# Optimization experiments

Measured on AMD Instinct MI355X. Metric: run time of the kernel, lower is better.

Reference implementation:

```python
import jax, jax.numpy as jnp
import numpy as np

MIN_DIST = 4
BASE_PRIMES = np.array([2, 3, 5, 7])  # A, C, G, U
# canonical pair prime products: AU=2*7=14, CG=3*5=15, GU=5*7=35


def nussinov(s):
    """Nussinov max-score non-crossing pairing: O(N^3) DP (vectorized per
    anti-diagonal) + stack-based traceback. s: [N,N] float64, symmetric, >=0.
    Returns symmetric 0/1 pair mask. Mirrors kirigami.nussinov (CPU numpy)."""
    N = s.shape[0]
    D = np.zeros((N, N))  # D[d, i] = dp[i, i+d]
    E = np.zeros((N, N))  # E[d, j] = dp[j-d, j]
    ar = np.arange(N)
    for d in range(1, N):
        m = N - d
        pair = (D[d - 2, 1:m + 1] if d >= 2 else 0.0) + s[ar[:m], ar[:m] + d]
        # split over k=i..j-1: dp[i,k] + dp[k+1,j] (k=i covers i-unpaired)
        split = (D[0:d, 0:m] + E[d - 1::-1, d:N]).max(axis=0)
        val = np.maximum(pair, split)
        D[d, :m] = val
        E[d, d:] = val
    dp = np.zeros((N, N))
    for d in range(1, N):
        dp[ar[:N - d], ar[:N - d] + d] = D[d, :N - d]
    eps = 1e-9
    pm = np.zeros((N, N))
    stack = [(0, N - 1)]
    while stack:
        i, j = stack.pop()
        if j <= i:
            continue
        v = dp[i, j]
        if v <= eps:
            continue
        if dp[i + 1, j] >= v - eps:
            stack.append((i + 1, j))
        elif s[i, j] > 0 and dp[i + 1, j - 1] + s[i, j] >= v - eps:
            pm[i, j] = pm[j, i] = 1.0
            stack.append((i + 1, j - 1))
        else:
            ks = np.arange(i, j)
            k = int(ks[np.argmax(dp[i, ks] + dp[ks + 1, j])])
            stack.append((i, k))
            stack.append((k + 1, j))
    return pm


def _premask(con, feat):
    """Symmetrize + remove sharp angles (tril(-4)+triu(4)) + canonical-pair mask."""
    c = con[0, 0]                      # [N, N]
    c = (c + c.T) * 0.5                # Symmetrize
    N = c.shape[0]
    idx = jnp.arange(N)
    dist_ok = jnp.abs(idx[:, None] - idx[None, :]) >= MIN_DIST  # RemoveSharp
    seq = feat[0, :4, :, 0]            # [4, N] one-hot base encoding
    primes = jnp.asarray(BASE_PRIMES)[jnp.argmax(seq, axis=0)]  # [N]
    prod = primes[:, None] * primes[None, :]
    canon = (prod == 14) | (prod == 15) | (prod == 35)          # Canonicalize
    return c * (dist_ok & canon)


def setup_inputs() -> dict:
    key = jax.random.key(0)
    k1, k2 = jax.random.split(key)
    N = 1024
    con = jax.random.uniform(k1, (1, 1, N, N), dtype=jnp.float32)
    feat = jax.random.normal(k2, (1, 16, N, N), dtype=jnp.float32)
    return {"con": con, "feat": feat}


def reference(con, feat):
    c = _premask(con, feat)
    # original: GPU->CPU numpy float64 DP, then mask back on device
    mask = nussinov(np.asarray(c, dtype=np.float64))
    out = c * jnp.asarray(mask, dtype=c.dtype)
    return out.reshape(con.shape)
```

## Files before the change

### kernel.cpp

```cpp
#include <hip/hip_runtime.h>

#define NN 1024
#define BT 32
#define TT 32
#define NTILES ((TT * (TT + 1)) / 2)

__device__ __forceinline__ double gload_cc(const double* p) {
    double v;
    asm volatile("global_load_dwordx2 %0, %1, off sc0 sc1" : "=v"(v) : "v"(p));
    return v;
}
__device__ __forceinline__ void gstore_cc(double* p, double v) {
    asm volatile("global_store_dwordx2 %0, %1, off sc0 sc1" :: "v"(p), "v"(v));
}
__device__ __forceinline__ void gstore_flag(int* p, int v) {
    asm volatile("global_store_dword %0, %1, off sc0 sc1" :: "v"(p), "v"(v));
}
#define VWAIT0 asm volatile("s_waitcnt vmcnt(0)" ::: "memory")

__device__ __forceinline__ void waitflag2(const int* f, int a0, int b0, int a1, int b1) {
    const int* p0 = &f[(a0 * TT + b0) << 4];
    const int* p1 = &f[(a1 * TT + b1) << 4];
    int it = 0;
    while (true) {
        int v0, v1;
        asm volatile("global_load_dword %0, %2, off sc0 sc1\n\t"
                     "global_load_dword %1, %3, off sc0 sc1\n\t"
                     "s_waitcnt vmcnt(0)"
                     : "=&v"(v0), "=&v"(v1)
                     : "v"(p0), "v"(p1));
        if (v0 & v1) break;
        if (it < 8) __builtin_amdgcn_s_sleep(1);
        else        __builtin_amdgcn_s_sleep(15);
        ++it;
    }
    asm volatile("" ::: "memory");
}
__device__ __forceinline__ void waitflag4(const int* f, int a0, int b0, int a1, int b1,
                                          int a2, int b2, int a3, int b3) {
    const int* p0 = &f[(a0 * TT + b0) << 4];
    const int* p1 = &f[(a1 * TT + b1) << 4];
    const int* p2 = &f[(a2 * TT + b2) << 4];
    const int* p3 = &f[(a3 * TT + b3) << 4];
    int it = 0;
    while (true) {
        int v0, v1, v2, v3;
        asm volatile("global_load_dword %0, %4, off sc0 sc1\n\t"
                     "global_load_dword %1, %5, off sc0 sc1\n\t"
                     "global_load_dword %2, %6, off sc0 sc1\n\t"
                     "global_load_dword %3, %7, off sc0 sc1\n\t"
                     "s_waitcnt vmcnt(0)"
                     : "=&v"(v0), "=&v"(v1), "=&v"(v2), "=&v"(v3)
                     : "v"(p0), "v"(p1), "v"(p2), "v"(p3));
        if (v0 & v1 & v2 & v3) break;
        if (it < 8) __builtin_amdgcn_s_sleep(1);
        else        __builtin_amdgcn_s_sleep(15);
        ++it;
    }
    asm volatile("" ::: "memory");
}
__device__ __forceinline__ void waitflag2_blk(const int* f, int a0, int b0, int a1, int b1) {
    if (threadIdx.x < 64) waitflag2(f, a0, b0, a1, b1);
    __syncthreads();
}
__device__ __forceinline__ void waitflag4_blk(const int* f, int a0, int b0, int a1, int b1,
                                              int a2, int b2, int a3, int b3) {
    if (threadIdx.x < 64) waitflag4(f, a0, b0, a1, b1, a2, b2, a3, b3);
    __syncthreads();
}

__global__ void primes_kernel(const float* __restrict__ feat, int* __restrict__ primes) {
    int i = blockIdx.x * blockDim.x + threadIdx.x;
    if (i < NN) {
        float best = feat[i * NN];
        int arg = 0;
        for (int ch = 1; ch < 4; ++ch) {
            float v = feat[ch * NN * NN + i * NN];
            if (v > best) { best = v; arg = ch; }
        }
        const int P[4] = {2, 3, 5, 7};
        primes[i] = P[arg];
    }
}

__global__ void prep_kernel(const float* __restrict__ con, const int* __restrict__ primes,
                            float* __restrict__ S, double* __restrict__ R,
                            double* __restrict__ C, float* __restrict__ out,
                            int* __restrict__ flags,
                            int* __restrict__ qi, int* __restrict__ qj,
                            int* __restrict__ qready, int* __restrict__ qctl) {
    int idx = blockIdx.x * blockDim.x + threadIdx.x;
    int i = idx >> 10;
    int j = idx & (NN - 1);
    float c = (con[idx] + con[j * NN + i]) * 0.5f;
    int prod = primes[i] * primes[j];
    bool canon = (prod == 14) | (prod == 15) | (prod == 35);
    int d = i - j; if (d < 0) d = -d;
    S[idx] = (canon && d >= 4) ? c : 0.0f;
    R[idx] = 0.0;
    C[idx] = 0.0;
    out[idx] = 0.0f;
    if (idx < TT * TT * 16) flags[idx] = 0;
    if (idx < 4096) qready[idx] = (idx == 0) ? 1 : 0;
    if (idx == 0) {
        qi[0] = 0; qj[0] = NN - 1;
        qctl[0] = 0;
        qctl[16] = 1;
        qctl[32] = 1;
    }
}

__global__ __launch_bounds__(256) void nuss_tiles_kernel(double* __restrict__ R,
                                                         double* __restrict__ C,
                                                         const float* __restrict__ S,
                                                         int* __restrict__ flags) {
    __shared__ double DJJc[32][33];
    __shared__ double Vtc[32][33];
    __shared__ __attribute__((aligned(16))) double Ast[32][34];
    __shared__ __attribute__((aligned(16))) double Bst[32][34];
    __shared__ double Pld[32][33];
    __shared__ float  Sld[32][32];
    __shared__ double edgeCol[33];
    __shared__ double Prt[2][4][32];

    int b = blockIdx.x, dd = 0;
    while (b >= TT - dd) { b -= TT - dd; ++dd; }
    const int I = b, J = b + dd;
    const int aI = I * BT, aJ = J * BT;
    const int tid = threadIdx.x;
    const int wid = tid >> 6;
    const int lane = tid & 63;
    const int r = lane >> 1;
    const int h = lane & 1;

    if (dd == 0) {
        #pragma unroll
        for (int w = 0; w < 4; ++w) {
            int idx = w * 256 + tid; int rr = idx >> 5, cc = idx & 31;
            Sld[rr][cc] = S[(aI + rr) * NN + aI + cc];
        }
        for (int idx = tid; idx < 32 * 33; idx += 256)
            ((double*)Vtc)[idx] = 0.0;
        __syncthreads();
        if (wid == 0) {
            double vrow[16];
            #pragma unroll
            for (int u = 0; u < 16; ++u) vrow[u] = 0.0;
            for (int s = 1; s <= 31; ++s) {
                int c = r + s;
                bool act = (c <= 31);
                double acc = 0.0;
                if (act) {
                    double t0 = 0.0, t1 = 0.0, t2 = 0.0, t3 = 0.0;
                    #pragma unroll
                    for (int u = 0; u < 16; u += 4) {
                        int k0 = h * 16 + u;
                        t0 = fmax(t0, vrow[u]     + Vtc[c][k0 + 1]);
                        t1 = fmax(t1, vrow[u + 1] + Vtc[c][k0 + 2]);
                        t2 = fmax(t2, vrow[u + 2] + Vtc[c][k0 + 3]);
                        t3 = fmax(t3, vrow[u + 3] + Vtc[c][k0 + 4]);
                    }
                    acc = fmax(fmax(t0, t1), fmax(t2, t3));
                }
                acc = fmax(acc, __shfl_xor(acc, 1));
                if (act) {
                    double best = fmax(acc, Vtc[c - 1][r + 1] + (double)Sld[r][c]);
                    if (h == 0) Vtc[c][r] = best;
                    #pragma unroll
                    for (int u = 0; u < 16; ++u)
                        if (h * 16 + u == c) vrow[u] = best;
                }
            }
        }
        __syncthreads();
        #pragma unroll
        for (int w = 0; w < 4; ++w) {
            int idx = w * 256 + tid; int rr = idx >> 5, cc = idx & 31;
            gstore_cc(&R[(aI + rr) * NN + aI + cc], Vtc[cc][rr]);
        }
        #pragma unroll
        for (int w = 0; w < 4; ++w) {
            int idx = w * 256 + tid; int cc = idx >> 5, rr = idx & 31;
            gstore_cc(&C[(aI + cc) * NN + aI + rr], Vtc[cc][rr]);
        }
        VWAIT0;
        __syncthreads();
        if (tid == 0) gstore_flag(&flags[(I * TT + I) << 4], 1);
        return;
    }

    const int nk = dd - 1;
    const int off = (wid & 1) * 16 + h * 8;
    waitflag2_blk(flags, I, I, J, J);

    double ra[4], rb[4];
    double ec = 0.0, ve = 0.0;
    double asl[8];
    double ar1 = 0.0;
    #pragma unroll
    for (int w = 0; w < 4; ++w) {
        int idx = w * 256 + tid; int cc = idx >> 5, mm = idx & 31;
        ra[w] = gload_cc(&C[(aJ + cc) * NN + aJ + mm]);
    }
    if (wid < 2) {
        #pragma unroll
        for (int u = 0; u < 8; ++u)
            asl[u] = gload_cc(&R[(aI + r) * NN + aI + off + u]);
    }
    if (r < 31) ar1 = gload_cc(&R[(aI + r) * NN + aI + r + 1]);
    if (wid == 0 && nk == 0) {
        if (lane < 33) ec = gload_cc(&R[(aI + lane) * NN + (aJ - 1)]);
        if (lane < 32) ve = gload_cc(&R[(aI + 32) * NN + aJ + lane]);
    }
    #pragma unroll
    for (int w = 0; w < 4; ++w) {
        int idx = w * 256 + tid; int rr = idx >> 5, cc = idx & 31;
        Sld[rr][cc] = S[(aI + rr) * NN + aJ + cc];
    }
    for (int idx = tid; idx < 32 * 33; idx += 256)
        ((double*)Vtc)[idx] = 0.0;
    VWAIT0;
    #pragma unroll
    for (int w = 0; w < 4; ++w) {
        int idx = w * 256 + tid; int cc = idx >> 5, mm = idx & 31;
        DJJc[cc][mm] = ra[w];
    }
    if (tid < 32) DJJc[tid][32] = 0.0;
    double slice8[8];
    if (wid < 2) {
        #pragma unroll
        for (int u = 0; u < 8; ++u)
            slice8[u] = (off + u > r + 1) ? asl[u] : -1.0e30;
    } else {
        #pragma unroll
        for (int u = 0; u < 8; ++u) slice8[u] = 0.0;
    }
    if (wid == 0 && nk == 0) {
        if (lane < 33) edgeCol[lane] = ec;
        if (lane < 32) Vtc[lane][32] = ve;
    }
    __syncthreads();

    double P[16];
    #pragma unroll
    for (int x = 0; x < 16; ++x) P[x] = 0.0;
    const int rg = lane >> 3, cg = lane & 7;
    const int r4 = rg * 4, c4 = cg * 4;

    auto kkloop = [&]() {
        for (int kk = wid * 8; kk < wid * 8 + 8; ++kk) {
            double2 av0 = *(const double2*)&Ast[kk][r4];
            double2 av1 = *(const double2*)&Ast[kk][r4 + 2];
            double2 bv0 = *(const double2*)&Bst[kk][c4];
            double2 bv1 = *(const double2*)&Bst[kk][c4 + 2];
            P[0]  = fmax(P[0],  av0.x + bv0.x); P[1]  = fmax(P[1],  av0.x + bv0.y);
            P[2]  = fmax(P[2],  av0.x + bv1.x); P[3]  = fmax(P[3],  av0.x + bv1.y);
            P[4]  = fmax(P[4],  av0.y + bv0.x); P[5]  = fmax(P[5],  av0.y + bv0.y);
            P[6]  = fmax(P[6],  av0.y + bv1.x); P[7]  = fmax(P[7],  av0.y + bv1.y);
            P[8]  = fmax(P[8],  av1.x + bv0.x); P[9]  = fmax(P[9],  av1.x + bv0.y);
            P[10] = fmax(P[10], av1.x + bv1.x); P[11] = fmax(P[11], av1.x + bv1.y);
            P[12] = fmax(P[12], av1.y + bv0.x); P[13] = fmax(P[13], av1.y + bv0.y);
            P[14] = fmax(P[14], av1.y + bv1.x); P[15] = fmax(P[15], av1.y + bv1.y);
        }
    };
    auto proc = [&](int t1, int t2, bool last) {
        if (t2 >= 0) waitflag4_blk(flags, I, t1, t1, J, I, t2, t2, J);
        else         waitflag2_blk(flags, I, t1, t1, J);
        if (last && wid == 0) {
            if (lane < 33) ec = gload_cc(&R[(aI + lane) * NN + (aJ - 1)]);
            if (lane < 32) ve = gload_cc(&R[(aI + 32) * NN + aJ + lane]);
        }
        int k1 = t1 * BT;
        #pragma unroll
        for (int w = 0; w < 4; ++w) {
            int idx = w * 256 + tid; int rr = idx >> 5, kk = idx & 31;
            ra[w] = gload_cc(&R[(aI + rr) * NN + k1 + kk]);
            rb[w] = gload_cc(&C[(aJ + rr) * NN + k1 + 1 + kk]);
        }
        VWAIT0;
        #pragma unroll
        for (int w = 0; w < 4; ++w) {
            int idx = w * 256 + tid; int rr = idx >> 5, kk = idx & 31;
            Ast[kk][rr] = ra[w];
            Bst[kk][rr] = rb[w];
        }
        if (last && wid == 0) {
            if (lane < 33) edgeCol[lane] = ec;
            if (lane < 32) Vtc[lane][32] = ve;
        }
        __syncthreads();
        if (t2 >= 0) {
            int k2 = t2 * BT;
            #pragma unroll
            for (int w = 0; w < 4; ++w) {
                int idx = w * 256 + tid; int rr = idx >> 5, kk = idx & 31;
                ra[w] = gload_cc(&R[(aI + rr) * NN + k2 + kk]);
                rb[w] = gload_cc(&C[(aJ + rr) * NN + k2 + 1 + kk]);
            }
        }
        kkloop();
        if (t2 >= 0) {
            __syncthreads();
            VWAIT0;
            #pragma unroll
            for (int w = 0; w < 4; ++w) {
                int idx = w * 256 + tid; int rr = idx >> 5, kk = idx & 31;
                Ast[kk][rr] = ra[w];
                Bst[kk][rr] = rb[w];
            }
            __syncthreads();
            kkloop();
        }
        __syncthreads();
    };

    {
        int tl = (I + J) >> 1, tr = ((I + J) >> 1) + 1;
        int pend = -1;
        for (int q = 0; q < nk; ++q) {
            int t;
            if ((q & 1) == 0) { if (tl >= I + 1) t = tl--; else t = tr++; }
            else              { if (tr <= J - 1) t = tr++; else t = tl--; }
            if (pend < 0) { pend = t; continue; }
            int rp = (pend - I > J - pend) ? pend - I : J - pend;
            int rt = (t - I > J - t) ? t - I : J - t;
            if (rp == rt) { proc(pend, t, q == nk - 1); pend = -1; }
            else          { proc(pend, -1, false); pend = t; }
        }
        if (pend >= 0) proc(pend, -1, true);
    }

    if (nk > 0) {
        if (wid == 0) {
            #pragma unroll
            for (int x = 0; x < 4; ++x)
                #pragma unroll
                for (int y = 0; y < 4; ++y)
                    Pld[r4 + x][c4 + y] = P[x * 4 + y];
        }
        __syncthreads();
        if (wid == 1) {
            #pragma unroll
            for (int x = 0; x < 4; ++x)
                #pragma unroll
                for (int y = 0; y < 4; ++y)
                    Pld[r4 + x][c4 + y] = fmax(Pld[r4 + x][c4 + y], P[x * 4 + y]);
        }
        __syncthreads();
        if (wid == 2) {
            #pragma unroll
            for (int x = 0; x < 4; ++x)
                #pragma unroll
                for (int y = 0; y < 4; ++y)
                    Pld[r4 + x][c4 + y] = fmax(Pld[r4 + x][c4 + y], P[x * 4 + y]);
        }
        __syncthreads();
        if (wid == 3) {
            #pragma unroll
            for (int x = 0; x < 4; ++x)
                #pragma unroll
                for (int y = 0; y < 4; ++y)
                    Pld[r4 + x][c4 + y] = fmax(Pld[r4 + x][c4 + y], P[x * 4 + y]);
        }
        __syncthreads();
    } else {
        for (int idx = tid; idx < 32 * 33; idx += 256)
            ((double*)Pld)[idx] = 0.0;
        __syncthreads();
    }

    {
        const double* bsel = (wid < 2) ? &Vtc[0][0] : &DJJc[0][0];
        double ecr = edgeCol[r];
        double ecp = edgeCol[r + 1];
        double pA[8], pB[8];
        double p1 = 0.0, p2 = 0.0, shc = 0.0, shp = 0.0, erc = 0.0, erp = 0.0;

#define PREFQ(PV, SS)                                                 \
    { int cq_ = (r + (SS) - 31) & 31;                                 \
      const double* bp_ = bsel + cq_ * 33 + off + 1;                  \
      _Pragma("unroll")                                               \
      for (int u = 0; u < 8; ++u) PV[u] = bp_[u]; }

#define STEPQ(PV, SS, BUF)                                            \
    { int c_ = r + (SS) - 31;                                         \
      bool act_ = ((unsigned)c_ < 32u);                               \
      int cc_ = c_ & 31;                                              \
      double t0_ = fmax(slice8[0] + PV[0], slice8[1] + PV[1]);        \
      double t1_ = fmax(slice8[2] + PV[2], slice8[3] + PV[3]);        \
      double t2_ = fmax(slice8[4] + PV[4], slice8[5] + PV[5]);        \
      double t3_ = fmax(slice8[6] + PV[6], slice8[7] + PV[7]);        \
      double pa_ = fmax(fmax(t0_, t1_), fmax(t2_, t3_));              \
      pa_ = fmax(pa_, __shfl_xor(pa_, 1));                            \
      if (h == 0) Prt[BUF][wid][r] = pa_;                             \
      __syncthreads();                                                \
      double a0_ = Prt[BUF][0][r];                                    \
      double a1_ = Prt[BUF][1][r];                                    \
      double a2_ = Prt[BUF][2][r];                                    \
      double a3_ = Prt[BUF][3][r];                                    \
      double er_  = Vtc[cc_][32];                                     \
      double dj0_ = DJJc[cc_][0];                                     \
      double pld_ = Pld[r][cc_];                                      \
      float  sld_ = Sld[r][cc_];                                      \
      shp = shc; erp = erc; erc = er_;                                \
      shc = __shfl_down(p1, 2);                                       \
      double shd_ = __shfl_down(p2, 4);                               \
      p2 = p1;                                                        \
      double acc_ = fmax(fmax(a0_, a1_), fmax(a2_, a3_));             \
      if (act_) {                                                     \
          double best_ = acc_;                                        \
          best_ = fmax(best_, (r == 31) ? erc : shc);                 \
          if (r < 31)                                                 \
              best_ = fmax(best_, ar1 + ((r == 30) ? erc : shd_));    \
          best_ = fmax(best_, ecr + dj0_);                            \
          best_ = fmax(best_, pld_);                                  \
          double pv_ = (c_ == 0) ? ecp : ((r == 31) ? erp : shp);     \
          best_ = fmax(best_, pv_ + (double)sld_);                    \
          if (wid == 0 && h == 0) Vtc[c_][r] = best_;                 \
          if (wid >= 2) {                                             \
              _Pragma("unroll")                                       \
              for (int u = 0; u < 8; ++u)                             \
                  if (off + u == c_) slice8[u] = best_;               \
          }                                                           \
          p1 = best_;                                                 \
      } }

        PREFQ(pA, 0)
        PREFQ(pB, 1)
        for (int s2 = 0; s2 < 64; s2 += 2) {
            STEPQ(pA, s2, 0)
            PREFQ(pA, s2 + 2)
            STEPQ(pB, s2 + 1, 1)
            PREFQ(pB, s2 + 3)
        }
#undef PREFQ
#undef STEPQ
    }
    __syncthreads();

    #pragma unroll
    for (int w = 0; w < 4; ++w) {
        int idx = w * 256 + tid; int rr = idx >> 5, cc = idx & 31;
        gstore_cc(&R[(aI + rr) * NN + aJ + cc], Vtc[cc][rr]);
    }
    #pragma unroll
    for (int w = 0; w < 4; ++w) {
        int idx = w * 256 + tid; int cc = idx >> 5, rr = idx & 31;
        gstore_cc(&C[(aJ + cc) * NN + aI + rr], Vtc[cc][rr]);
    }
    VWAIT0;
    __syncthreads();
    if (tid == 0) gstore_flag(&flags[(I * TT + J) << 4], 1);
}

__global__ __launch_bounds__(256) void traceback_kernel(const double* __restrict__ R,
                                                        const double* __restrict__ C,
                                                        const float* __restrict__ S,
                                                        float* __restrict__ out,
                                                        int* __restrict__ qi,
                                                        int* __restrict__ qj,
                                                        int* __restrict__ qready,
                                                        int* __restrict__ qctl) {
    __shared__ double Rw[16][17];
    __shared__ float  Sw[16][17];
    __shared__ int sh_cmd, sh_i, sh_j;
    __shared__ double sred_v[4];
    __shared__ int sred_k[4];
    const double eps = 1e-9;
    const int tid = threadIdx.x;
    int* headp = qctl;
    int* tailp = qctl + 16;
    int* pendp = qctl + 32;

    int i = 0, j = 0; double v = 0.0;
    bool have = false;
    int ai = -(1 << 29), aj = 0;
    int myidx = -1;

    while (true) {
        if (tid == 0) {
            int cmd;
            int guard = 0;
            while (true) {
                if (!have) {
                    if (++guard > (1 << 22)) { cmd = -1; break; }
                    if (myidx < 0) myidx = atomicAdd(headp, 1);
                    int rdy = 0;
                    if (myidx < 4096)
                        rdy = __hip_atomic_load(&qready[myidx], __ATOMIC_RELAXED,
                                                __HIP_MEMORY_SCOPE_AGENT);
                    if (rdy) {
                        int ni, nj;
                        asm volatile("global_load_dword %0, %2, off sc0 sc1\n\t"
                                     "global_load_dword %1, %3, off sc0 sc1\n\t"
                                     "s_waitcnt vmcnt(0)"
                                     : "=&v"(ni), "=&v"(nj)
                                     : "v"(&qi[myidx]), "v"(&qj[myidx]));
                        myidx = -1;
                        i = ni; j = nj;
                        if (j <= i) { atomicAdd(pendp, -1); continue; }
                        v = R[i * NN + j];
                        if (v <= eps) { atomicAdd(pendp, -1); continue; }
                        have = true;
                        continue;
                    }
                    int pend = __hip_atomic_load(pendp, __ATOMIC_RELAXED,
                                                 __HIP_MEMORY_SCOPE_AGENT);
                    if (pend == 0) { cmd = -1; break; }
                    __builtin_amdgcn_s_sleep(2);
                    continue;
                }
                int u = i - ai, w = aj - j;
                if ((unsigned)u > 15u || (unsigned)w > 14u) { cmd = 1; break; }
                double a = Rw[u][w];
                if (a >= v - eps) {
                    ++i; v = a;
                    if (j <= i || v <= eps) { have = false; atomicAdd(pendp, -1); }
                    continue;
                }
                float sv = Sw[u][w];
                double b2 = Rw[u][w + 1];
                if (sv > 0.0f && b2 + (double)sv >= v - eps) {
                    out[i * NN + j] = sv; out[j * NN + i] = sv;
                    ++i; --j; v = b2;
                    if (j <= i || v <= eps) { have = false; atomicAdd(pendp, -1); }
                    continue;
                }
                cmd = 0; break;
            }
            sh_cmd = cmd; sh_i = i; sh_j = j;
        }
        __syncthreads();
        int cmd = sh_cmd;
        if (cmd < 0) break;

        if (cmd == 1) {
            int i0 = sh_i, j0 = sh_j;
            int di = tid >> 4, dj = tid & 15;
            int rr = i0 + 1 + di; if (rr > NN - 1) rr = NN - 1;
            int cc = j0 - dj;     if (cc < 0) cc = 0;
            Rw[di][dj] = R[rr * NN + cc];
            int sr = i0 + di;     if (sr > NN - 1) sr = NN - 1;
            Sw[di][dj] = S[sr * NN + cc];
            __syncthreads();
            if (tid == 0) { ai = i0; aj = j0; }
            continue;
        }

        const int si = sh_i, sj = sh_j;
        double bv = -1.0; int bk = 0x7fffffff;
        for (int k = si + tid; k < sj; k += 256) {
            double tv = R[si * NN + k] + C[sj * NN + k + 1];
            if (tv > bv) { bv = tv; bk = k; }
        }
        for (int offr = 32; offr; offr >>= 1) {
            double ov = __shfl_down(bv, offr);
            int    ok = __shfl_down(bk, offr);
            if (ov > bv || (ov == bv && ok < bk)) { bv = ov; bk = ok; }
        }
        if ((tid & 63) == 0) { sred_v[tid >> 6] = bv; sred_k[tid >> 6] = bk; }
        __syncthreads();
        if (tid == 0) {
            double fv = sred_v[0]; int fk = sred_k[0];
            for (int w = 1; w < 4; ++w)
                if (sred_v[w] > fv || (sred_v[w] == fv && sred_k[w] < fk)) { fv = sred_v[w]; fk = sred_k[w]; }
            int slot = atomicAdd(tailp, 1);
            int rv = fk + 1;
            asm volatile("global_store_dword %0, %1, off sc0 sc1" :: "v"(&qi[slot]), "v"(rv));
            asm volatile("global_store_dword %0, %1, off sc0 sc1" :: "v"(&qj[slot]), "v"(sj));
            VWAIT0;
            atomicAdd(pendp, 1);
            VWAIT0;
            gstore_flag(&qready[slot], 1);
            j = fk;
            if (j <= i) { have = false; atomicAdd(pendp, -1); }
            else {
                v = R[i * NN + j];
                if (v <= eps) { have = false; atomicAdd(pendp, -1); }
                else have = true;
            }
        }
        __syncthreads();
    }
}

extern "C" void kernel_launch(void* const* d_in, const int* in_sizes, int n_in,
                              void* d_out, int out_size, void* d_ws, size_t ws_size,
                              hipStream_t stream) {
    const float* con  = (const float*)d_in[0];
    const float* feat = (const float*)d_in[1];
    float* out = (float*)d_out;

    char* ws = (char*)d_ws;
    double* R      = (double*)(ws);
    double* C      = (double*)(ws + (size_t)8  * 1024 * 1024);
    float*  S      = (float*) (ws + (size_t)16 * 1024 * 1024);
    int*    primes = (int*)   (ws + (size_t)20 * 1024 * 1024);
    int*    flags  = (int*)   (ws + (size_t)20 * 1024 * 1024 + 8192);
    char*   qbase  = ws + (size_t)20 * 1024 * 1024 + 128 * 1024;
    int*    qi     = (int*)(qbase);
    int*    qj     = (int*)(qbase + 16 * 1024);
    int*    qready = (int*)(qbase + 32 * 1024);
    int*    qctl   = (int*)(qbase + 48 * 1024);

    primes_kernel<<<(NN + 255) / 256, 256, 0, stream>>>(feat, primes);
    prep_kernel<<<(NN * NN) / 256, 256, 0, stream>>>(con, primes, S, R, C, out, flags,
                                                     qi, qj, qready, qctl);
    nuss_tiles_kernel<<<NTILES, 256, 0, stream>>>(R, C, S, flags);
    traceback_kernel<<<64, 256, 0, stream>>>(R, C, S, out, qi, qj, qready, qctl);
}
```

Measured before the change: 1.141 ms.

## Pipeline diagonal partial reductions two steps ahead with triple-buffered shared scratch

Restructures the per-tile anti-diagonal wavefront so each step's partial max over the split terms is computed and written to a triple-buffered shared array two steps before it is consumed. The barrier sits at the end of each step instead of between the partial write and its read. This is meant to take the reduction arithmetic off the serial critical path. It also adds a dj1 term using p2 to handle nearby split candidates that the lookahead partials cannot yet see, and flattens the max chain into a tree. The price is a more complex dependency scheme that could be wrong if the lookahead misses any just-computed value.

```diff
diff --git a/kernel.cpp b/kernel.cpp
--- a/kernel.cpp
+++ b/kernel.cpp
@@ -121,7 +121,7 @@
     __shared__ double Pld[32][33];
     __shared__ float  Sld[32][32];
     __shared__ double edgeCol[33];
-    __shared__ double Prt[2][4][32];
+    __shared__ __attribute__((aligned(16))) double Prt[3][32][6];
 
     int b = blockIdx.x, dd = 0;
     while (b >= TT - dd) { b -= TT - dd; ++dd; }
@@ -373,68 +373,74 @@
         const double* bsel = (wid < 2) ? &Vtc[0][0] : &DJJc[0][0];
         double ecr = edgeCol[r];
         double ecp = edgeCol[r + 1];
-        double pA[8], pB[8];
+        double pv[8];
         double p1 = 0.0, p2 = 0.0, shc = 0.0, shp = 0.0, erc = 0.0, erp = 0.0;
 
-#define PREFQ(PV, SS)                                                 \
+#define PREFQ(SS)                                                     \
     { int cq_ = (r + (SS) - 31) & 31;                                 \
       const double* bp_ = bsel + cq_ * 33 + off + 1;                  \
       _Pragma("unroll")                                               \
-      for (int u = 0; u < 8; ++u) PV[u] = bp_[u]; }
-
-#define STEPQ(PV, SS, BUF)                                            \
+      for (int u = 0; u < 8; ++u) pv[u] = bp_[u]; }
+
+#define PARTQ(SS)                                                     \
+    { double t0_ = fmax(slice8[0] + pv[0], slice8[1] + pv[1]);        \
+      double t1_ = fmax(slice8[2] + pv[2], slice8[3] + pv[3]);        \
+      double t2_ = fmax(slice8[4] + pv[4], slice8[5] + pv[5]);        \
+      double t3_ = fmax(slice8[6] + pv[6], slice8[7] + pv[7]);        \
+      double pa_ = fmax(fmax(t0_, t1_), fmax(t2_, t3_));              \
+      pa_ = fmax(pa_, __shfl_xor(pa_, 1));                            \
+      if (h == 0) Prt[(SS) % 3][r][wid] = pa_; }
+
+#define STEPB(SS)                                                     \
     { int c_ = r + (SS) - 31;                                         \
       bool act_ = ((unsigned)c_ < 32u);                               \
       int cc_ = c_ & 31;                                              \
-      double t0_ = fmax(slice8[0] + PV[0], slice8[1] + PV[1]);        \
-      double t1_ = fmax(slice8[2] + PV[2], slice8[3] + PV[3]);        \
-      double t2_ = fmax(slice8[4] + PV[4], slice8[5] + PV[5]);        \
-      double t3_ = fmax(slice8[6] + PV[6], slice8[7] + PV[7]);        \
-      double pa_ = fmax(fmax(t0_, t1_), fmax(t2_, t3_));              \
-      pa_ = fmax(pa_, __shfl_xor(pa_, 1));                            \
-      if (h == 0) Prt[BUF][wid][r] = pa_;                             \
-      __syncthreads();                                                \
-      double a0_ = Prt[BUF][0][r];                                    \
-      double a1_ = Prt[BUF][1][r];                                    \
-      double a2_ = Prt[BUF][2][r];                                    \
-      double a3_ = Prt[BUF][3][r];                                    \
+      double a0_ = Prt[(SS) % 3][r][0];                               \
+      double a1_ = Prt[(SS) % 3][r][1];                               \
+      double a2_ = Prt[(SS) % 3][r][2];                               \
+      double a3_ = Prt[(SS) % 3][r][3];                               \
       double er_  = Vtc[cc_][32];                                     \
       double dj0_ = DJJc[cc_][0];                                     \
+      double dj1_ = DJJc[cc_][(cc_ > 0) ? cc_ - 1 : 0];               \
       double pld_ = Pld[r][cc_];                                      \
       float  sld_ = Sld[r][cc_];                                      \
       shp = shc; erp = erc; erc = er_;                                \
       shc = __shfl_down(p1, 2);                                       \
       double shd_ = __shfl_down(p2, 4);                               \
-      p2 = p1;                                                        \
       double acc_ = fmax(fmax(a0_, a1_), fmax(a2_, a3_));             \
       if (act_) {                                                     \
-          double best_ = acc_;                                        \
-          best_ = fmax(best_, (r == 31) ? erc : shc);                 \
-          if (r < 31)                                                 \
-              best_ = fmax(best_, ar1 + ((r == 30) ? erc : shd_));    \
-          best_ = fmax(best_, ecr + dj0_);                            \
-          best_ = fmax(best_, pld_);                                  \
+          double b0_ = fmax(acc_, (r == 31) ? erc : shc);             \
+          double b1_ = (r < 31) ? (ar1 + ((r == 30) ? erc : shd_))    \
+                                : -1.0e30;                            \
+          double b2_ = fmax(p1, p2 + dj1_);                           \
+          double b3_ = fmax(ecr + dj0_, pld_);                        \
           double pv_ = (c_ == 0) ? ecp : ((r == 31) ? erp : shp);     \
-          best_ = fmax(best_, pv_ + (double)sld_);                    \
+          double b4_ = fmax(pv_ + (double)sld_, b1_);                 \
+          double best_ = fmax(fmax(b0_, b2_), fmax(b3_, b4_));        \
           if (wid == 0 && h == 0) Vtc[c_][r] = best_;                 \
           if (wid >= 2) {                                             \
               _Pragma("unroll")                                       \
               for (int u = 0; u < 8; ++u)                             \
                   if (off + u == c_) slice8[u] = best_;               \
           }                                                           \
-          p1 = best_;                                                 \
-      } }
-
-        PREFQ(pA, 0)
-        PREFQ(pB, 1)
-        for (int s2 = 0; s2 < 64; s2 += 2) {
-            STEPQ(pA, s2, 0)
-            PREFQ(pA, s2 + 2)
-            STEPQ(pB, s2 + 1, 1)
-            PREFQ(pB, s2 + 3)
+          p2 = p1; p1 = best_;                                        \
+      } else { p2 = p1; }                                             \
+      __syncthreads(); }
+
+        PREFQ(0) PARTQ(0)
+        PREFQ(1) PARTQ(1)
+        __syncthreads();
+        for (int s3 = 0; s3 < 63; s3 += 3) {
+            PREFQ(s3 + 2) PARTQ(s3 + 2)
+            STEPB(s3)
+            PREFQ(s3 + 3) PARTQ(s3 + 3)
+            STEPB(s3 + 1)
+            PREFQ(s3 + 4) PARTQ(s3 + 4)
+            STEPB(s3 + 2)
         }
 #undef PREFQ
-#undef STEPQ
+#undef PARTQ
+#undef STEPB
     }
     __syncthreads();
 
```

Result: slower. 1.180 ms (+3.4%).

## Fuse traceback into DP tile kernel, gated on final tile flag

Applied to the files above, without the earlier changes.

Moves the traceback work into extra blocks appended to the DP tile kernel grid. These blocks spin on the flag of the last tile (0,31) and then run the same queue-based traceback. This removes one kernel launch and the boundary between the two kernels. The traceback blocks share LDS with the tile code by aliasing the tile buffers, which could lower occupancy, and their spinning could compete with the DP blocks for compute units. The prep kernel also zeroes R and C with double2 stores instead of scalar stores.

```diff
diff --git a/kernel.cpp b/kernel.cpp
--- a/kernel.cpp
+++ b/kernel.cpp
@@ -4,6 +4,7 @@
 #define BT 32
 #define TT 32
 #define NTILES ((TT * (TT + 1)) / 2)
+#define TBBLK 64
 
 __device__ __forceinline__ double gload_cc(const double* p) {
     double v;
@@ -97,9 +98,11 @@
     bool canon = (prod == 14) | (prod == 15) | (prod == 35);
     int d = i - j; if (d < 0) d = -d;
     S[idx] = (canon && d >= 4) ? c : 0.0f;
-    R[idx] = 0.0;
-    C[idx] = 0.0;
     out[idx] = 0.0f;
+    if (idx < NN * NN / 2) {
+        ((double2*)R)[idx] = make_double2(0.0, 0.0);
+        ((double2*)C)[idx] = make_double2(0.0, 0.0);
+    }
     if (idx < TT * TT * 16) flags[idx] = 0;
     if (idx < 4096) qready[idx] = (idx == 0) ? 1 : 0;
     if (idx == 0) {
@@ -110,10 +113,15 @@
     }
 }
 
-__global__ __launch_bounds__(256) void nuss_tiles_kernel(double* __restrict__ R,
+__global__ __launch_bounds__(256) void nuss_fused_kernel(double* __restrict__ R,
                                                          double* __restrict__ C,
                                                          const float* __restrict__ S,
-                                                         int* __restrict__ flags) {
+                                                         int* __restrict__ flags,
+                                                         float* __restrict__ out,
+                                                         int* __restrict__ qi,
+                                                         int* __restrict__ qj,
+                                                         int* __restrict__ qready,
+                                                         int* __restrict__ qctl) {
     __shared__ double DJJc[32][33];
     __shared__ double Vtc[32][33];
     __shared__ __attribute__((aligned(16))) double Ast[32][34];
@@ -123,13 +131,154 @@
     __shared__ double edgeCol[33];
     __shared__ double Prt[2][4][32];
 
+    const int tid = threadIdx.x;
+    const int wid = tid >> 6;
+    const int lane = tid & 63;
+
+    if (blockIdx.x >= NTILES) {
+        double (*Rw)[17] = (double(*)[17])&DJJc[0][0];
+        float  (*Sw)[17] = (float (*)[17])&Vtc[0][0];
+        int*    shctl    = (int*)&Pld[0][0];
+        double* sredv    = &Pld[2][0];
+        int*    sredk    = (int*)&Pld[4][0];
+        const double eps = 1e-9;
+        int* headp = qctl;
+        int* tailp = qctl + 16;
+        int* pendp = qctl + 32;
+
+        if (tid == 0) {
+            const int* fr = &flags[(0 * TT + 31) << 4];
+            int it = 0;
+            while (true) {
+                int v0;
+                asm volatile("global_load_dword %0, %1, off sc0 sc1\n\t"
+                             "s_waitcnt vmcnt(0)" : "=&v"(v0) : "v"(fr));
+                if (v0) break;
+                if (it < 8) __builtin_amdgcn_s_sleep(1);
+                else        __builtin_amdgcn_s_sleep(15);
+                ++it;
+            }
+            asm volatile("" ::: "memory");
+        }
+        __syncthreads();
+
+        int i = 0, j = 0; double v = 0.0;
+        bool have = false;
+        int ai = -(1 << 29), aj = 0;
+        int myidx = -1;
+
+        while (true) {
+            if (tid == 0) {
+                int cmd;
+                int guard = 0;
+                while (true) {
+                    if (!have) {
+                        if (++guard > (1 << 22)) { cmd = -1; break; }
+                        if (myidx < 0) myidx = atomicAdd(headp, 1);
+                        int rdy = 0;
+                        if (myidx < 4096)
+                            rdy = __hip_atomic_load(&qready[myidx], __ATOMIC_RELAXED,
+                                                    __HIP_MEMORY_SCOPE_AGENT);
+                        if (rdy) {
+                            int ni, nj;
+                            asm volatile("global_load_dword %0, %2, off sc0 sc1\n\t"
+                                         "global_load_dword %1, %3, off sc0 sc1\n\t"
+                                         "s_waitcnt vmcnt(0)"
+                                         : "=&v"(ni), "=&v"(nj)
+                                         : "v"(&qi[myidx]), "v"(&qj[myidx]));
+                            myidx = -1;
+                            i = ni; j = nj;
+                            if (j <= i) { atomicAdd(pendp, -1); continue; }
+                            v = R[i * NN + j];
+                            if (v <= eps) { atomicAdd(pendp, -1); continue; }
+                            have = true;
+                            continue;
+                        }
+                        int pend = __hip_atomic_load(pendp, __ATOMIC_RELAXED,
+                                                     __HIP_MEMORY_SCOPE_AGENT);
+                        if (pend == 0) { cmd = -1; break; }
+                        __builtin_amdgcn_s_sleep(2);
+                        continue;
+                    }
+                    int u = i - ai, w = aj - j;
+                    if ((unsigned)u > 15u || (unsigned)w > 14u) { cmd = 1; break; }
+                    double a = Rw[u][w];
+                    if (a >= v - eps) {
+                        ++i; v = a;
+                        if (j <= i || v <= eps) { have = false; atomicAdd(pendp, -1); }
+                        continue;
+                    }
+                    float sv = Sw[u][w];
+                    double b2 = Rw[u][w + 1];
+                    if (sv > 0.0f && b2 + (double)sv >= v - eps) {
+                        out[i * NN + j] = sv; out[j * NN + i] = sv;
+                        ++i; --j; v = b2;
+                        if (j <= i || v <= eps) { have = false; atomicAdd(pendp, -1); }
+                        continue;
+                    }
+                    cmd = 0; break;
+                }
+                shctl[0] = cmd; shctl[1] = i; shctl[2] = j;
+            }
+            __syncthreads();
+            int cmd = shctl[0];
+            if (cmd < 0) break;
+
+            if (cmd == 1) {
+                int i0 = shctl[1], j0 = shctl[2];
+                int di = tid >> 4, dj = tid & 15;
+                int rr = i0 + 1 + di; if (rr > NN - 1) rr = NN - 1;
+                int cc = j0 - dj;     if (cc < 0) cc = 0;
+                Rw[di][dj] = R[rr * NN + cc];
+                int sr = i0 + di;     if (sr > NN - 1) sr = NN - 1;
+                Sw[di][dj] = S[sr * NN + cc];
+                __syncthreads();
+                if (tid == 0) { ai = i0; aj = j0; }
+                continue;
+            }
+
+            const int si = shctl[1], sj = shctl[2];
+            double bv = -1.0; int bk = 0x7fffffff;
+            for (int k = si + tid; k < sj; k += 256) {
+                double tv = R[si * NN + k] + C[sj * NN + k + 1];
+                if (tv > bv) { bv = tv; bk = k; }
+            }
+            for (int offr = 32; offr; offr >>= 1) {
+                double ov = __shfl_down(bv, offr);
+                int    ok = __shfl_down(bk, offr);
+                if (ov > bv || (ov == bv && ok < bk)) { bv = ov; bk = ok; }
+            }
+            if ((tid & 63) == 0) { sredv[tid >> 6] = bv; sredk[tid >> 6] = bk; }
+            __syncthreads();
+            if (tid == 0) {
+                double fv = sredv[0]; int fk = sredk[0];
+                for (int w = 1; w < 4; ++w)
+                    if (sredv[w] > fv || (sredv[w] == fv && sredk[w] < fk)) { fv = sredv[w]; fk = sredk[w]; }
+                int slot = atomicAdd(tailp, 1);
+                int rv = fk + 1;
+                asm volatile("global_store_dword %0, %1, off sc0 sc1" :: "v"(&qi[slot]), "v"(rv));
+                asm volatile("global_store_dword %0, %1, off sc0 sc1" :: "v"(&qj[slot]), "v"(sj));
+                VWAIT0;
+                atomicAdd(pendp, 1);
+                VWAIT0;
+                gstore_flag(&qready[slot], 1);
+                j = fk;
+                if (j <= i) { have = false; atomicAdd(pendp, -1); }
+                else {
+                    v = R[i * NN + j];
+                    if (v <= eps) { have = false; atomicAdd(pendp, -1); }
+                    else have = true;
+                }
+            }
+            __syncthreads();
+        }
+        return;
+    }
+
     int b = blockIdx.x, dd = 0;
     while (b >= TT - dd) { b -= TT - dd; ++dd; }
     const int I = b, J = b + dd;
     const int aI = I * BT, aJ = J * BT;
-    const int tid = threadIdx.x;
-    const int wid = tid >> 6;
-    const int lane = tid & 63;
     const int r = lane >> 1;
     const int h = lane & 1;
 
@@ -453,137 +602,6 @@
     if (tid == 0) gstore_flag(&flags[(I * TT + J) << 4], 1);
 }
 
-__global__ __launch_bounds__(256) void traceback_kernel(const double* __restrict__ R,
-                                                        const double* __restrict__ C,
-                                                        const float* __restrict__ S,
-                                                        float* __restrict__ out,
-                                                        int* __restrict__ qi,
-                                                        int* __restrict__ qj,
-                                                        int* __restrict__ qready,
-                                                        int* __restrict__ qctl) {
-    __shared__ double Rw[16][17];
-    __shared__ float  Sw[16][17];
-    __shared__ int sh_cmd, sh_i, sh_j;
-    __shared__ double sred_v[4];
-    __shared__ int sred_k[4];
-    const double eps = 1e-9;
-    const int tid = threadIdx.x;
-    int* headp = qctl;
-    int* tailp = qctl + 16;
-    int* pendp = qctl + 32;
-
-    int i = 0, j = 0; double v = 0.0;
-    bool have = false;
-    int ai = -(1 << 29), aj = 0;
-    int myidx = -1;
-
-    while (true) {
-        if (tid == 0) {
-            int cmd;
-            int guard = 0;
-            while (true) {
-                if (!have) {
-                    if (++guard > (1 << 22)) { cmd = -1; break; }
-                    if (myidx < 0) myidx = atomicAdd(headp, 1);
-                    int rdy = 0;
-                    if (myidx < 4096)
-                        rdy = __hip_atomic_load(&qready[myidx], __ATOMIC_RELAXED,
-                                                __HIP_MEMORY_SCOPE_AGENT);
-                    if (rdy) {
-                        int ni, nj;
-                        asm volatile("global_load_dword %0, %2, off sc0 sc1\n\t"
-                                     "global_load_dword %1, %3, off sc0 sc1\n\t"
-                                     "s_waitcnt vmcnt(0)"
-                                     : "=&v"(ni), "=&v"(nj)
-                                     : "v"(&qi[myidx]), "v"(&qj[myidx]));
-                        myidx = -1;
-                        i = ni; j = nj;
-                        if (j <= i) { atomicAdd(pendp, -1); continue; }
-                        v = R[i * NN + j];
-                        if (v <= eps) { atomicAdd(pendp, -1); continue; }
-                        have = true;
-                        continue;
-                    }
-                    int pend = __hip_atomic_load(pendp, __ATOMIC_RELAXED,
-                                                 __HIP_MEMORY_SCOPE_AGENT);
-                    if (pend == 0) { cmd = -1; break; }
-                    __builtin_amdgcn_s_sleep(2);
-                    continue;
-                }
-                int u = i - ai, w = aj - j;
-                if ((unsigned)u > 15u || (unsigned)w > 14u) { cmd = 1; break; }
-                double a = Rw[u][w];
-                if (a >= v - eps) {
-                    ++i; v = a;
-                    if (j <= i || v <= eps) { have = false; atomicAdd(pendp, -1); }
-                    continue;
-                }
-                float sv = Sw[u][w];
-                double b2 = Rw[u][w + 1];
-                if (sv > 0.0f && b2 + (double)sv >= v - eps) {
-                    out[i * NN + j] = sv; out[j * NN + i] = sv;
-                    ++i; --j; v = b2;
-                    if (j <= i || v <= eps) { have = false; atomicAdd(pendp, -1); }
-                    continue;
-                }
-                cmd = 0; break;
-            }
-            sh_cmd = cmd; sh_i = i; sh_j = j;
-        }
-        __syncthreads();
-        int cmd = sh_cmd;
-        if (cmd < 0) break;
-
-        if (cmd == 1) {
-            int i0 = sh_i, j0 = sh_j;
-            int di = tid >> 4, dj = tid & 15;
-            int rr = i0 + 1 + di; if (rr > NN - 1) rr = NN - 1;
-            int cc = j0 - dj;     if (cc < 0) cc = 0;
-            Rw[di][dj] = R[rr * NN + cc];
-            int sr = i0 + di;     if (sr > NN - 1) sr = NN - 1;
-            Sw[di][dj] = S[sr * NN + cc];
-            __syncthreads();
-            if (tid == 0) { ai = i0; aj = j0; }
-            continue;
-        }
-
-        const int si = sh_i, sj = sh_j;
-        double bv = -1.0; int bk = 0x7fffffff;
-        for (int k = si + tid; k < sj; k += 256) {
-            double tv = R[si * NN + k] + C[sj * NN + k + 1];
-            if (tv > bv) { bv = tv; bk = k; }
-        }
-        for (int offr = 32; offr; offr >>= 1) {
-            double ov = __shfl_down(bv, offr);
-            int    ok = __shfl_down(bk, offr);
-            if (ov > bv || (ov == bv && ok < bk)) { bv = ov; bk = ok; }
-        }
-        if ((tid & 63) == 0) { sred_v[tid >> 6] = bv; sred_k[tid >> 6] = bk; }
-        __syncthreads();
-        if (tid == 0) {
-            double fv = sred_v[0]; int fk = sred_k[0];
-            for (int w = 1; w < 4; ++w)
-                if (sred_v[w] > fv || (sred_v[w] == fv && sred_k[w] < fk)) { fv = sred_v[w]; fk = sred_k[w]; }
-            int slot = atomicAdd(tailp, 1);
-            int rv = fk + 1;
-            asm volatile("global_store_dword %0, %1, off sc0 sc1" :: "v"(&qi[slot]), "v"(rv));
-            asm volatile("global_store_dword %0, %1, off sc0 sc1" :: "v"(&qj[slot]), "v"(sj));
-            VWAIT0;
-            atomicAdd(pendp, 1);
-            VWAIT0;
-            gstore_flag(&qready[slot], 1);
-            j = fk;
-            if (j <= i) { have = false; atomicAdd(pendp, -1); }
-            else {
-                v = R[i * NN + j];
-                if (v <= eps) { have = false; atomicAdd(pendp, -1); }
-                else have = true;
-            }
-        }
-        __syncthreads();
-    }
-}
-
 extern "C" void kernel_launch(void* const* d_in, const int* in_sizes, int n_in,
                               void* d_out, int out_size, void* d_ws, size_t ws_size,
                               hipStream_t stream) {
@@ -606,6 +624,6 @@
     primes_kernel<<<(NN + 255) / 256, 256, 0, stream>>>(feat, primes);
     prep_kernel<<<(NN * NN) / 256, 256, 0, stream>>>(con, primes, S, R, C, out, flags,
                                                      qi, qj, qready, qctl);
-    nuss_tiles_kernel<<<NTILES, 256, 0, stream>>>(R, C, S, flags);
-    traceback_kernel<<<64, 256, 0, stream>>>(R, C, S, out, qi, qj, qready, qctl);
-}
+    nuss_fused_kernel<<<NTILES + TBBLK, 256, 0, stream>>>(R, C, S, flags, out,
+                                                          qi, qj, qready, qctl);
+}
```

After: 1.130 ms. No clear change (-1.0%).
